# Performance work log

Hardware: AMD Instinct MI355X
Metric: run time of the kernel (lower is better)

Reference implementation:

```python
import jax, jax.numpy as jnp
import numpy as np

B, S, D, H = 2, 2048, 1024, 16
DK = D // H


def setup_inputs() -> dict:
    key = jax.random.key(0)
    ks = jax.random.split(key, 7)
    q = jax.random.normal(ks[0], (B, S, D), dtype=jnp.float32)
    k = jax.random.normal(ks[1], (B, S, D), dtype=jnp.float32)
    v = jax.random.normal(ks[2], (B, S, D), dtype=jnp.float32)
    # causal mask, broadcastable [B,1,S,S]; masked_fill where mask==0
    mask = jnp.broadcast_to(jnp.tril(jnp.ones((S, S), dtype=jnp.int32)), (B, 1, S, S))
    scale = 0.02
    Wq = jax.random.normal(ks[3], (D, D), dtype=jnp.float32) * scale
    Wk = jax.random.normal(ks[4], (D, D), dtype=jnp.float32) * scale
    Wv = jax.random.normal(ks[5], (D, D), dtype=jnp.float32) * scale
    Wo = jax.random.normal(ks[6], (D, D), dtype=jnp.float32) * scale
    return {"q": q, "k": k, "v": v, "mask": mask, "Wq": Wq, "Wk": Wk, "Wv": Wv, "Wo": Wo}


def reference(q, k, v, mask, Wq, Wk, Wv, Wo):
    # torch nn.Linear(bias=False): y = x @ W.T with W of shape [out, in]
    def proj(x, W):
        return (x @ W.T).reshape(B, S, H, DK).transpose(0, 2, 1, 3)  # [B,H,S,DK]

    Q = proj(q, Wq)
    K = proj(k, Wk)
    V = proj(v, Wv)
    inv_sqrt_dk = np.float32(1.0 / np.sqrt(DK))
    scores = jnp.einsum('bhqd,bhkd->bhqk', Q, K) * inv_sqrt_dk  # [B,H,S,S]
    scores = jnp.where(mask == 0, jnp.float32(-jnp.inf), scores)
    attn = jax.nn.softmax(scores, axis=-1)
    x = jnp.einsum('bhqk,bhkd->bhqd', attn, V)  # [B,H,S,DK]
    x = x.transpose(0, 2, 1, 3).reshape(B, S, D)
    return x @ Wo.T
```

## Files before the change

kernel.cpp:

```cpp
#include <hip/hip_runtime.h>

typedef __bf16 bf16x8 __attribute__((ext_vector_type(8)));
typedef __bf16 bf16x2 __attribute__((ext_vector_type(2)));
typedef float  f32x4  __attribute__((ext_vector_type(4)));

#define DEV static __device__ __forceinline__
#define VMCNT(n) asm volatile("s_waitcnt vmcnt(" #n ")" ::: "memory")
#define LGKM0()  asm volatile("s_waitcnt lgkmcnt(0)" ::: "memory")
#define SBAR()   __builtin_amdgcn_s_barrier()
#define SFENCE() __builtin_amdgcn_sched_barrier(0)


DEV ushort f2bf(float f) {
    return __builtin_bit_cast(ushort, (__bf16)f);
}
DEV uint pk2(float a, float b) {
    bf16x2 t; t[0] = (__bf16)a; t[1] = (__bf16)b;
    return __builtin_bit_cast(uint, t);
}

DEV float redmax4(float x) {
    x = fmaxf(x, __shfl_xor(x, 16));
    return fmaxf(x, __shfl_xor(x, 32));
}
DEV float redsum4(float x) {
    x += __shfl_xor(x, 16);
    return x + __shfl_xor(x, 32);
}

DEV void stage_swz(const ushort* g, int gstride, char* lds, int nchunks) {
    const int tid  = threadIdx.x;
    const int lane = tid & 63;
    const int wave = tid >> 6;
    for (int c0 = wave * 64; c0 < nchunks; c0 += 256) {
        int c   = c0 + lane;
        int row = c >> 3;
        int cc  = (c & 7) ^ (row & 7);
        const ushort* src = g + row * gstride + cc * 8;
        __builtin_amdgcn_global_load_lds((__attribute__((address_space(1))) void*)src,
                                         (__attribute__((address_space(3))) void*)(lds + c0 * 16),
                                         16, 0, 0);
    }
}

DEV void stage_swz32(const float* g, int gstride, char* lds, int nchunks) {
    const int tid  = threadIdx.x;
    const int lane = tid & 63;
    const int wave = tid >> 6;
    for (int c0 = wave * 64; c0 < nchunks; c0 += 256) {
        int c   = c0 + lane;
        int row = c >> 4;
        int cc  = (c & 15) ^ (row & 15);
        const float* src = g + row * gstride + cc * 4;
        __builtin_amdgcn_global_load_lds((__attribute__((address_space(1))) void*)src,
                                         (__attribute__((address_space(3))) void*)(lds + c0 * 16),
                                         16, 0, 0);
    }
}

DEV bf16x8 ldfrag(const char* tile, int row, int kc) {
    int off = (row << 7) + ((kc ^ (row & 7)) << 4);
    return *(const bf16x8*)(tile + off);
}

DEV bf16x8 ldfrag32(const char* tile, int row, int cl0) {
    const int base = row << 8, rs = row & 15;
    f32x4 v0 = *(const f32x4*)(tile + base + ((cl0 ^ rs) << 4));
    f32x4 v1 = *(const f32x4*)(tile + base + (((cl0 + 1) ^ rs) << 4));
    uint4 u;
    u.x = pk2(v0[0], v0[1]); u.y = pk2(v0[2], v0[3]);
    u.z = pk2(v1[0], v1[1]); u.w = pk2(v1[2], v1[3]);
    return __builtin_bit_cast(bf16x8, u);
}


struct CvtArgs { const float* s[4]; ushort* d[4]; int n; };

__global__ void cvt_kernel(CvtArgs a) {
    const float* __restrict__ s = a.s[blockIdx.y];
    ushort* __restrict__ d = a.d[blockIdx.y];
    const int stride = gridDim.x * blockDim.x;
    for (int i = blockIdx.x * blockDim.x + threadIdx.x; i * 8 < a.n; i += stride) {
        const float4* p = (const float4*)(s + (size_t)i * 8);
        float4 x = p[0], yv = p[1];
        uint4 o;
        o.x = pk2(x.x,  x.y);
        o.y = pk2(x.z,  x.w);
        o.z = pk2(yv.x, yv.y);
        o.w = pk2(yv.z, yv.w);
        *(uint4*)(d + (size_t)i * 8) = o;
    }
}

constexpr int GN = 1024, GK = 1024;


struct ProjArgs {
    const float* A[3]; const ushort* W[3]; ushort* O[3];
    float scale[3]; int mode[3];
};

__global__ __launch_bounds__(256, 3) void gemm_proj(ProjArgs args) {
    __shared__ char smem[49152];
    const int z = blockIdx.z;
    const float* A = args.A[z];
    const ushort* W = args.W[z];
    ushort* Out = args.O[z];
    const float scale = args.scale[z];
    const int mode = args.mode[z];

    const int tid  = threadIdx.x;
    const int lane = tid & 63;
    const int w    = tid >> 6;
    const int wr   = w >> 1, wc = w & 1;
    const int hi   = lane >> 4, lj = lane & 15;
    const int g    = blockIdx.x;
    const int o_   = ((g & 7) << 5) | (g >> 3);
    const int nb   = o_ & 7, mb = o_ >> 3;

    f32x4 acc[4][4];
#pragma unroll
    for (int mi = 0; mi < 4; mi++)
#pragma unroll
        for (int ni = 0; ni < 4; ni++) acc[mi][ni] = f32x4{0.f, 0.f, 0.f, 0.f};

    const float*  Ag = A + (size_t)mb * 128 * GK;
    const ushort* Wg = W + (size_t)nb * 128 * GK;

    for (int k0 = 0; k0 < GK; k0 += 64) {
        __syncthreads();
        stage_swz32(Ag + k0, GK, smem, 2048);
        stage_swz(Wg + k0, GK, smem + 32768, 1024);
        __syncthreads();
#pragma unroll
        for (int kk = 0; kk < 2; ++kk) {
            bf16x8 a[4], b[4];
#pragma unroll
            for (int mi = 0; mi < 4; mi++) a[mi] = ldfrag32(smem, wr * 64 + mi * 16 + lj, kk * 8 + hi * 2);
#pragma unroll
            for (int ni = 0; ni < 4; ni++) b[ni] = ldfrag(smem + 32768, wc * 64 + ni * 16 + lj, kk * 4 + hi);
#pragma unroll
            for (int mi = 0; mi < 4; mi++)
#pragma unroll
                for (int ni = 0; ni < 4; ni++)
                    acc[mi][ni] = __builtin_amdgcn_mfma_f32_16x16x32_bf16(a[mi], b[ni], acc[mi][ni], 0, 0, 0);
        }
    }

#pragma unroll
    for (int mi = 0; mi < 4; mi++)
#pragma unroll
        for (int r = 0; r < 4; r++) {
            const int gm = mb * 128 + wr * 64 + mi * 16 + hi * 4 + r;
            const int b_ = gm >> 11, s_ = gm & 2047;
#pragma unroll
            for (int ni = 0; ni < 4; ni++) {
                const int gn = nb * 128 + wc * 64 + ni * 16 + lj;
                const int h_ = gn >> 6, d_ = gn & 63;
                float v = acc[mi][ni][r] * scale;
                size_t off;
                if (mode == 0) off = (((size_t)b_ * 16 + h_) * 2048 + s_) * 64 + d_;
                else           off = (((size_t)b_ * 16 + h_) * 64 + d_) * 2048 + s_;
                Out[off] = f2bf(v);
            }
        }
}


__global__ __launch_bounds__(256, 3) void gemm_out(const ushort* __restrict__ A,
                                                   const ushort* __restrict__ W,
                                                   float* __restrict__ Out) {
    __shared__ char smem[32768];
    const int tid  = threadIdx.x;
    const int lane = tid & 63;
    const int w    = tid >> 6;
    const int wr   = w >> 1, wc = w & 1;
    const int hi   = lane >> 4, lj = lane & 15;
    const int g    = blockIdx.x;
    const int o_   = ((g & 7) << 5) | (g >> 3);
    const int nb   = o_ & 7, mb = o_ >> 3;

    f32x4 acc[4][4];
#pragma unroll
    for (int mi = 0; mi < 4; mi++)
#pragma unroll
        for (int ni = 0; ni < 4; ni++) acc[mi][ni] = f32x4{0.f, 0.f, 0.f, 0.f};

    const ushort* Ag = A + (size_t)mb * 128 * GK;
    const ushort* Wg = W + (size_t)nb * 128 * GK;

    for (int k0 = 0; k0 < GK; k0 += 64) {
        __syncthreads();
        stage_swz(Ag + k0, GK, smem, 1024);
        stage_swz(Wg + k0, GK, smem + 16384, 1024);
        __syncthreads();
#pragma unroll
        for (int kk = 0; kk < 2; ++kk) {
            bf16x8 a[4], b[4];
#pragma unroll
            for (int mi = 0; mi < 4; mi++) a[mi] = ldfrag(smem, wr * 64 + mi * 16 + lj, kk * 4 + hi);
#pragma unroll
            for (int ni = 0; ni < 4; ni++) b[ni] = ldfrag(smem + 16384, wc * 64 + ni * 16 + lj, kk * 4 + hi);
#pragma unroll
            for (int mi = 0; mi < 4; mi++)
#pragma unroll
                for (int ni = 0; ni < 4; ni++)
                    acc[mi][ni] = __builtin_amdgcn_mfma_f32_16x16x32_bf16(a[mi], b[ni], acc[mi][ni], 0, 0, 0);
        }
    }

#pragma unroll
    for (int mi = 0; mi < 4; mi++)
#pragma unroll
        for (int r = 0; r < 4; r++) {
            const int gm = mb * 128 + wr * 64 + mi * 16 + hi * 4 + r;
#pragma unroll
            for (int ni = 0; ni < 4; ni++) {
                const int gn = nb * 128 + wc * 64 + ni * 16 + lj;
                Out[(size_t)gm * GN + gn] = acc[mi][ni][r];
            }
        }
}


__global__ __launch_bounds__(256, 3) void attn_kernel(const ushort* __restrict__ Qb,
                                                      const ushort* __restrict__ Kb,
                                                      const ushort* __restrict__ Vt,
                                                      ushort* __restrict__ Xb,
                                                      ushort* __restrict__ Opart,
                                                      float* __restrict__ Mlp) {
    constexpr int S = 2048;
    __shared__ char smem[49152];
    const int tid = threadIdx.x, lane = tid & 63, w = tid >> 6;
    const int hi = lane >> 4, lj = lane & 15;
    char* Pw = smem + 32768 + w * 4096;
    const int bh = blockIdx.x;
    const int y = blockIdx.y;

    int qt, slice, nsl;
    if (y < 16)      { qt = 12 + (y & 3);            slice = y >> 2;        nsl = 4; }
    else if (y < 28) { int zz = y - 16; qt = 8 + (zz & 3); slice = zz >> 2; nsl = 3; }
    else if (y < 36) { int zz = y - 28; qt = 4 + (zz & 3); slice = zz >> 2; nsl = 2; }
    else             { qt = y - 36;                  slice = 0;             nsl = 1; }
    const int nt  = 2 * qt + 2;
    const int kts = (nt * slice) / nsl;
    const int kte = (nt * (slice + 1)) / nsl;
    const bool partial = (nsl > 1);

    const int q0 = qt * 128;
    const int q0w = q0 + w * 32;

    const ushort* Qg = Qb + (size_t)bh * S * 64;
    const ushort* Kg = Kb + (size_t)bh * S * 64;
    const ushort* Vg = Vt + (size_t)bh * 64 * S;

    bf16x8 qf[2][2];
#pragma unroll
    for (int mi = 0; mi < 2; mi++)
#pragma unroll
        for (int kk = 0; kk < 2; kk++)
            qf[mi][kk] = *(const bf16x8*)(Qg + (size_t)(q0w + mi * 16 + lj) * 64 + kk * 32 + hi * 8);

    f32x4 o[2][4];
    float m_run[2] = { -1e30f, -1e30f }, l_run[2] = { 0.f, 0.f };
#pragma unroll
    for (int mi = 0; mi < 2; mi++)
#pragma unroll
        for (int nd = 0; nd < 4; nd++) o[mi][nd] = f32x4{0.f, 0.f, 0.f, 0.f};

    stage_swz(Kg + (size_t)kts * 64 * 64, 64, smem, 512);
    stage_swz(Vg + kts * 64, S, smem + 16384, 512);
    int cur = 0;

    for (int t = kts; t < kte; ++t) {
        char* Kc = smem + (cur << 13);
        char* Vc = smem + 16384 + (cur << 13);
        if (t + 1 < kte) {
            stage_swz(Kg + (size_t)(t + 1) * 64 * 64, 64, smem + ((cur ^ 1) << 13), 512);
            stage_swz(Vg + (t + 1) * 64, S, smem + 16384 + ((cur ^ 1) << 13), 512);
            VMCNT(4);
        } else {
            VMCNT(0);
        }
        SBAR(); SFENCE();

        if (t * 64 <= q0w + 31) {
            f32x4 sc[2][4];
#pragma unroll
            for (int mi = 0; mi < 2; mi++)
#pragma unroll
                for (int ni = 0; ni < 4; ni++) sc[mi][ni] = f32x4{0.f, 0.f, 0.f, 0.f};
            __builtin_amdgcn_s_setprio(1);
#pragma unroll
            for (int kk = 0; kk < 2; ++kk) {
                bf16x8 kf[4];
#pragma unroll
                for (int ni = 0; ni < 4; ni++) kf[ni] = ldfrag(Kc, ni * 16 + lj, kk * 4 + hi);
#pragma unroll
                for (int mi = 0; mi < 2; mi++)
#pragma unroll
                    for (int ni = 0; ni < 4; ni++)
                        sc[mi][ni] = __builtin_amdgcn_mfma_f32_16x16x32_bf16(kf[ni], qf[mi][kk], sc[mi][ni], 0, 0, 0);
            }
            __builtin_amdgcn_s_setprio(0);

            const bool diag = (t * 64 + 63 > q0w);
#pragma unroll
            for (int mi = 0; mi < 2; mi++) {
                const int q = q0w + mi * 16 + lj;
                if (diag) {
#pragma unroll
                    for (int ni = 0; ni < 4; ni++)
#pragma unroll
                        for (int r = 0; r < 4; r++)
                            if (t * 64 + ni * 16 + hi * 4 + r > q) sc[mi][ni][r] = -1e30f;
                }
                float mx = -1e30f;
#pragma unroll
                for (int ni = 0; ni < 4; ni++)
#pragma unroll
                    for (int r = 0; r < 4; r++) mx = fmaxf(mx, sc[mi][ni][r]);
                mx = redmax4(mx);
                const float mo = m_run[mi];
                const bool defer = __all(mx <= mo + 8.f);
                float mn, rs;
                if (defer) { mn = mo; rs = 1.f; }
                else { mn = fmaxf(mo, mx); rs = __builtin_exp2f(mo - mn); m_run[mi] = mn; }
                float ps = 0.f;
                const int row = mi * 16 + lj;
#pragma unroll
                for (int ni = 0; ni < 4; ni++) {
                    float p0 = __builtin_exp2f(sc[mi][ni][0] - mn);
                    float p1 = __builtin_exp2f(sc[mi][ni][1] - mn);
                    float p2 = __builtin_exp2f(sc[mi][ni][2] - mn);
                    float p3 = __builtin_exp2f(sc[mi][ni][3] - mn);
                    ps += (p0 + p1) + (p2 + p3);
                    uint2 pv; pv.x = pk2(p0, p1); pv.y = pk2(p2, p3);
                    const int c = ni * 2 + (hi >> 1);
                    *(uint2*)(Pw + row * 128 + ((c ^ (row & 7)) << 4) + ((hi & 1) << 3)) = pv;
                }
                ps = redsum4(ps);
                if (defer) {
                    l_run[mi] += ps;
                } else {
                    l_run[mi] = l_run[mi] * rs + ps;
#pragma unroll
                    for (int r = 0; r < 4; r++) {
                        float rr = __shfl(rs, (lane & 48) | (hi * 4 + r));
#pragma unroll
                        for (int nd = 0; nd < 4; nd++) o[mi][nd][r] *= rr;
                    }
                }
            }

            LGKM0(); SFENCE();

            __builtin_amdgcn_s_setprio(1);
#pragma unroll
            for (int kk = 0; kk < 2; ++kk) {
                bf16x8 pa[2], bv[4];
#pragma unroll
                for (int mi = 0; mi < 2; mi++) pa[mi] = ldfrag(Pw, mi * 16 + lj, kk * 4 + hi);
#pragma unroll
                for (int nd = 0; nd < 4; nd++) bv[nd] = ldfrag(Vc, nd * 16 + lj, kk * 4 + hi);
#pragma unroll
                for (int mi = 0; mi < 2; mi++)
#pragma unroll
                    for (int nd = 0; nd < 4; nd++)
                        o[mi][nd] = __builtin_amdgcn_mfma_f32_16x16x32_bf16(pa[mi], bv[nd], o[mi][nd], 0, 0, 0);
            }
            __builtin_amdgcn_s_setprio(0);
        }

        LGKM0();
        SBAR(); SFENCE();
        cur ^= 1;
    }

    if (partial) {
        const int pidx = bh * 40 + y;
        ushort* Op = Opart + (size_t)pidx * 8192;
        float*  Ml = Mlp   + (size_t)pidx * 256;
#pragma unroll
        for (int mi = 0; mi < 2; mi++)
#pragma unroll
            for (int r = 0; r < 4; r++) {
                const int row = w * 32 + mi * 16 + hi * 4 + r;
#pragma unroll
                for (int nd = 0; nd < 4; nd++)
                    Op[row * 64 + nd * 16 + lj] = f2bf(o[mi][nd][r]);
            }
        if (hi == 0) {
#pragma unroll
            for (int mi = 0; mi < 2; mi++) {
                const int row = w * 32 + mi * 16 + lj;
                Ml[row * 2 + 0] = m_run[mi];
                Ml[row * 2 + 1] = l_run[mi];
            }
        }
    } else {
        const int b_ = bh >> 4, h_ = bh & 15;
#pragma unroll
        for (int mi = 0; mi < 2; mi++)
#pragma unroll
            for (int r = 0; r < 4; r++) {
                float lv = __shfl(l_run[mi], (lane & 48) | (hi * 4 + r));
                float inv = 1.f / lv;
                const int srow = q0w + mi * 16 + hi * 4 + r;
#pragma unroll
                for (int nd = 0; nd < 4; nd++)
                    Xb[((size_t)b_ * S + srow) * 1024 + h_ * 64 + nd * 16 + lj] =
                        f2bf(o[mi][nd][r] * inv);
            }
    }
}


__global__ __launch_bounds__(256) void attn_merge(const ushort* __restrict__ Op,
                                                  const float* __restrict__ Ml,
                                                  ushort* __restrict__ Xb) {
    const int bh = blockIdx.x;
    const int qt = 4 + blockIdx.y;
    const int nsl  = (qt < 8) ? 2 : (qt < 12) ? 3 : 4;
    const int ybase = (qt >= 12) ? (qt - 12) : (qt >= 8) ? (16 + qt - 8) : (28 + qt - 4);
    const int tid = threadIdx.x;
    const int row = tid >> 1;
    const int c0 = (tid & 1) * 32;

    float ms[4], ls[4];
    float m = -1e30f;
    for (int s = 0; s < nsl; ++s) {
        const int slot = bh * 40 + ybase + s * 4;
        ms[s] = Ml[(size_t)slot * 256 + row * 2 + 0];
        ls[s] = Ml[(size_t)slot * 256 + row * 2 + 1];
        m = fmaxf(m, ms[s]);
    }
    float acc[32];
#pragma unroll
    for (int c = 0; c < 32; ++c) acc[c] = 0.f;
    float l = 0.f;
    for (int s = 0; s < nsl; ++s) {
        const float a = __builtin_exp2f(ms[s] - m);
        l += ls[s] * a;
        const ushort* op = Op + (size_t)(bh * 40 + ybase + s * 4) * 8192 + row * 64 + c0;
#pragma unroll
        for (int c8 = 0; c8 < 32; c8 += 8) {
            bf16x8 v = *(const bf16x8*)(op + c8);
#pragma unroll
            for (int e = 0; e < 8; ++e) acc[c8 + e] += a * (float)v[e];
        }
    }
    const float inv = 1.f / l;
    const int b_ = bh >> 4, h_ = bh & 15;
    ushort* dst = Xb + ((size_t)b_ * 2048 + qt * 128 + row) * 1024 + h_ * 64 + c0;
#pragma unroll
    for (int c = 0; c < 32; c += 2)
        *(uint*)(dst + c) = pk2(acc[c] * inv, acc[c + 1] * inv);
}


extern "C" void kernel_launch(void* const* d_in, const int* in_sizes, int n_in,
                              void* d_out, int out_size, void* d_ws, size_t ws_size,
                              hipStream_t stream) {
    (void)in_sizes; (void)n_in; (void)out_size; (void)ws_size;
    const float* q  = (const float*)d_in[0];
    const float* k  = (const float*)d_in[1];
    const float* v  = (const float*)d_in[2];
    const float* Wq = (const float*)d_in[4];
    const float* Wk = (const float*)d_in[5];
    const float* Wv = (const float*)d_in[6];
    const float* Wo = (const float*)d_in[7];

    char* ws = (char*)d_ws;
    const size_t MB = (size_t)1 << 20;
    ushort* Qb   = (ushort*)(ws + 0 * MB);
    ushort* Kb   = (ushort*)(ws + 8 * MB);
    ushort* Vtb  = (ushort*)(ws + 16 * MB);
    ushort* Xb   = (ushort*)(ws + 24 * MB);
    ushort* Wqb  = (ushort*)(ws + 32 * MB);
    ushort* Wkb  = (ushort*)(ws + 34 * MB);
    ushort* Wvb  = (ushort*)(ws + 36 * MB);
    ushort* Wob  = (ushort*)(ws + 38 * MB);
    ushort* Opart= (ushort*)(ws + 40 * MB);
    float*  Mlp  = (float*) (ws + 60 * MB);

    CvtArgs c;
    c.s[0] = Wq;  c.s[1] = Wk;  c.s[2] = Wv;  c.s[3] = Wo;
    c.d[0] = Wqb; c.d[1] = Wkb; c.d[2] = Wvb; c.d[3] = Wob;
    c.n = 1024 * 1024;
    cvt_kernel<<<dim3(512, 4), 256, 0, stream>>>(c);

    ProjArgs p;
    p.A[0] = q;   p.A[1] = k;   p.A[2] = v;
    p.W[0] = Wqb; p.W[1] = Wkb; p.W[2] = Wvb;
    p.O[0] = Qb;  p.O[1] = Kb;  p.O[2] = Vtb;
    p.scale[0] = 0.125f * 1.44269504088896f;
    p.scale[1] = 1.0f; p.scale[2] = 1.0f;
    p.mode[0] = 0; p.mode[1] = 0; p.mode[2] = 1;
    gemm_proj<<<dim3(256, 1, 3), 256, 0, stream>>>(p);

    attn_kernel<<<dim3(32, 40), 256, 0, stream>>>(Qb, Kb, Vtb, Xb, Opart, Mlp);
    attn_merge<<<dim3(32, 12), 256, 0, stream>>>(Opart, Mlp, Xb);

    gemm_out<<<256, 256, 0, stream>>>(Xb, Wob, (float*)d_out);
}
```

Baseline: 248.3 us.

## Pre-convert activations to bf16 and halve output GEMM N-tile

```diff
diff --git a/kernel.cpp b/kernel.cpp
--- a/kernel.cpp
+++ b/kernel.cpp
@@ -43,44 +43,21 @@
     }
 }
 
-DEV void stage_swz32(const float* g, int gstride, char* lds, int nchunks) {
-    const int tid  = threadIdx.x;
-    const int lane = tid & 63;
-    const int wave = tid >> 6;
-    for (int c0 = wave * 64; c0 < nchunks; c0 += 256) {
-        int c   = c0 + lane;
-        int row = c >> 4;
-        int cc  = (c & 15) ^ (row & 15);
-        const float* src = g + row * gstride + cc * 4;
-        __builtin_amdgcn_global_load_lds((__attribute__((address_space(1))) void*)src,
-                                         (__attribute__((address_space(3))) void*)(lds + c0 * 16),
-                                         16, 0, 0);
-    }
-}
-
 DEV bf16x8 ldfrag(const char* tile, int row, int kc) {
     int off = (row << 7) + ((kc ^ (row & 7)) << 4);
     return *(const bf16x8*)(tile + off);
 }
 
-DEV bf16x8 ldfrag32(const char* tile, int row, int cl0) {
-    const int base = row << 8, rs = row & 15;
-    f32x4 v0 = *(const f32x4*)(tile + base + ((cl0 ^ rs) << 4));
-    f32x4 v1 = *(const f32x4*)(tile + base + (((cl0 + 1) ^ rs) << 4));
-    uint4 u;
-    u.x = pk2(v0[0], v0[1]); u.y = pk2(v0[2], v0[3]);
-    u.z = pk2(v1[0], v1[1]); u.w = pk2(v1[2], v1[3]);
-    return __builtin_bit_cast(bf16x8, u);
-}
-
-
-struct CvtArgs { const float* s[4]; ushort* d[4]; int n; };
+
+struct CvtArgs { const float* s[7]; ushort* d[7]; int n[7]; };
 
 __global__ void cvt_kernel(CvtArgs a) {
-    const float* __restrict__ s = a.s[blockIdx.y];
-    ushort* __restrict__ d = a.d[blockIdx.y];
+    const int y = blockIdx.y;
+    const float* __restrict__ s = a.s[y];
+    ushort* __restrict__ d = a.d[y];
+    const int n = a.n[y];
     const int stride = gridDim.x * blockDim.x;
-    for (int i = blockIdx.x * blockDim.x + threadIdx.x; i * 8 < a.n; i += stride) {
+    for (int i = blockIdx.x * blockDim.x + threadIdx.x; i * 8 < n; i += stride) {
         const float4* p = (const float4*)(s + (size_t)i * 8);
         float4 x = p[0], yv = p[1];
         uint4 o;
@@ -96,14 +73,14 @@
 
 
 struct ProjArgs {
-    const float* A[3]; const ushort* W[3]; ushort* O[3];
+    const ushort* A[3]; const ushort* W[3]; ushort* O[3];
     float scale[3]; int mode[3];
 };
 
 __global__ __launch_bounds__(256, 3) void gemm_proj(ProjArgs args) {
-    __shared__ char smem[49152];
+    __shared__ char smem[32768];
     const int z = blockIdx.z;
-    const float* A = args.A[z];
+    const ushort* A = args.A[z];
     const ushort* W = args.W[z];
     ushort* Out = args.O[z];
     const float scale = args.scale[z];
@@ -124,21 +101,21 @@
 #pragma unroll
         for (int ni = 0; ni < 4; ni++) acc[mi][ni] = f32x4{0.f, 0.f, 0.f, 0.f};
 
-    const float*  Ag = A + (size_t)mb * 128 * GK;
+    const ushort* Ag = A + (size_t)mb * 128 * GK;
     const ushort* Wg = W + (size_t)nb * 128 * GK;
 
     for (int k0 = 0; k0 < GK; k0 += 64) {
         __syncthreads();
-        stage_swz32(Ag + k0, GK, smem, 2048);
-        stage_swz(Wg + k0, GK, smem + 32768, 1024);
+        stage_swz(Ag + k0, GK, smem, 1024);
+        stage_swz(Wg + k0, GK, smem + 16384, 1024);
         __syncthreads();
 #pragma unroll
         for (int kk = 0; kk < 2; ++kk) {
             bf16x8 a[4], b[4];
 #pragma unroll
-            for (int mi = 0; mi < 4; mi++) a[mi] = ldfrag32(smem, wr * 64 + mi * 16 + lj, kk * 8 + hi * 2);
-#pragma unroll
-            for (int ni = 0; ni < 4; ni++) b[ni] = ldfrag(smem + 32768, wc * 64 + ni * 16 + lj, kk * 4 + hi);
+            for (int mi = 0; mi < 4; mi++) a[mi] = ldfrag(smem, wr * 64 + mi * 16 + lj, kk * 4 + hi);
+#pragma unroll
+            for (int ni = 0; ni < 4; ni++) b[ni] = ldfrag(smem + 16384, wc * 64 + ni * 16 + lj, kk * 4 + hi);
 #pragma unroll
             for (int mi = 0; mi < 4; mi++)
 #pragma unroll
@@ -170,41 +147,41 @@
 __global__ __launch_bounds__(256, 3) void gemm_out(const ushort* __restrict__ A,
                                                    const ushort* __restrict__ W,
                                                    float* __restrict__ Out) {
-    __shared__ char smem[32768];
+    __shared__ char smem[24576];
     const int tid  = threadIdx.x;
     const int lane = tid & 63;
     const int w    = tid >> 6;
     const int wr   = w >> 1, wc = w & 1;
     const int hi   = lane >> 4, lj = lane & 15;
     const int g    = blockIdx.x;
-    const int o_   = ((g & 7) << 5) | (g >> 3);
-    const int nb   = o_ & 7, mb = o_ >> 3;
-
-    f32x4 acc[4][4];
+    const int o_   = ((g & 7) << 6) | (g >> 3);
+    const int nb   = o_ & 15, mb = o_ >> 4;
+
+    f32x4 acc[4][2];
 #pragma unroll
     for (int mi = 0; mi < 4; mi++)
 #pragma unroll
-        for (int ni = 0; ni < 4; ni++) acc[mi][ni] = f32x4{0.f, 0.f, 0.f, 0.f};
+        for (int ni = 0; ni < 2; ni++) acc[mi][ni] = f32x4{0.f, 0.f, 0.f, 0.f};
 
     const ushort* Ag = A + (size_t)mb * 128 * GK;
-    const ushort* Wg = W + (size_t)nb * 128 * GK;
+    const ushort* Wg = W + (size_t)nb * 64 * GK;
 
     for (int k0 = 0; k0 < GK; k0 += 64) {
         __syncthreads();
         stage_swz(Ag + k0, GK, smem, 1024);
-        stage_swz(Wg + k0, GK, smem + 16384, 1024);
+        stage_swz(Wg + k0, GK, smem + 16384, 512);
         __syncthreads();
 #pragma unroll
         for (int kk = 0; kk < 2; ++kk) {
-            bf16x8 a[4], b[4];
+            bf16x8 a[4], b[2];
 #pragma unroll
             for (int mi = 0; mi < 4; mi++) a[mi] = ldfrag(smem, wr * 64 + mi * 16 + lj, kk * 4 + hi);
 #pragma unroll
-            for (int ni = 0; ni < 4; ni++) b[ni] = ldfrag(smem + 16384, wc * 64 + ni * 16 + lj, kk * 4 + hi);
+            for (int ni = 0; ni < 2; ni++) b[ni] = ldfrag(smem + 16384, wc * 32 + ni * 16 + lj, kk * 4 + hi);
 #pragma unroll
             for (int mi = 0; mi < 4; mi++)
 #pragma unroll
-                for (int ni = 0; ni < 4; ni++)
+                for (int ni = 0; ni < 2; ni++)
                     acc[mi][ni] = __builtin_amdgcn_mfma_f32_16x16x32_bf16(a[mi], b[ni], acc[mi][ni], 0, 0, 0);
         }
     }
@@ -215,8 +192,8 @@
         for (int r = 0; r < 4; r++) {
             const int gm = mb * 128 + wr * 64 + mi * 16 + hi * 4 + r;
 #pragma unroll
-            for (int ni = 0; ni < 4; ni++) {
-                const int gn = nb * 128 + wc * 64 + ni * 16 + lj;
+            for (int ni = 0; ni < 2; ni++) {
+                const int gn = nb * 64 + wc * 32 + ni * 16 + lj;
                 Out[(size_t)gm * GN + gn] = acc[mi][ni][r];
             }
         }
@@ -477,21 +454,25 @@
     ushort* Kb   = (ushort*)(ws + 8 * MB);
     ushort* Vtb  = (ushort*)(ws + 16 * MB);
     ushort* Xb   = (ushort*)(ws + 24 * MB);
-    ushort* Wqb  = (ushort*)(ws + 32 * MB);
-    ushort* Wkb  = (ushort*)(ws + 34 * MB);
-    ushort* Wvb  = (ushort*)(ws + 36 * MB);
-    ushort* Wob  = (ushort*)(ws + 38 * MB);
-    ushort* Opart= (ushort*)(ws + 40 * MB);
-    float*  Mlp  = (float*) (ws + 60 * MB);
+    ushort* qb   = (ushort*)(ws + 32 * MB);
+    ushort* kb   = (ushort*)(ws + 40 * MB);
+    ushort* vb   = (ushort*)(ws + 48 * MB);
+    ushort* Wqb  = (ushort*)(ws + 56 * MB);
+    ushort* Wkb  = (ushort*)(ws + 58 * MB);
+    ushort* Wvb  = (ushort*)(ws + 60 * MB);
+    ushort* Wob  = (ushort*)(ws + 62 * MB);
+    ushort* Opart= (ushort*)(ws + 32 * MB);
+    float*  Mlp  = (float*) (ws + 52 * MB);
 
     CvtArgs c;
-    c.s[0] = Wq;  c.s[1] = Wk;  c.s[2] = Wv;  c.s[3] = Wo;
-    c.d[0] = Wqb; c.d[1] = Wkb; c.d[2] = Wvb; c.d[3] = Wob;
-    c.n = 1024 * 1024;
-    cvt_kernel<<<dim3(512, 4), 256, 0, stream>>>(c);
+    c.s[0] = q;  c.s[1] = k;  c.s[2] = v;  c.s[3] = Wq;  c.s[4] = Wk;  c.s[5] = Wv;  c.s[6] = Wo;
+    c.d[0] = qb; c.d[1] = kb; c.d[2] = vb; c.d[3] = Wqb; c.d[4] = Wkb; c.d[5] = Wvb; c.d[6] = Wob;
+    c.n[0] = c.n[1] = c.n[2] = 4 * 1024 * 1024;
+    c.n[3] = c.n[4] = c.n[5] = c.n[6] = 1024 * 1024;
+    cvt_kernel<<<dim3(1024, 7), 256, 0, stream>>>(c);
 
     ProjArgs p;
-    p.A[0] = q;   p.A[1] = k;   p.A[2] = v;
+    p.A[0] = qb;  p.A[1] = kb;  p.A[2] = vb;
     p.W[0] = Wqb; p.W[1] = Wkb; p.W[2] = Wvb;
     p.O[0] = Qb;  p.O[1] = Kb;  p.O[2] = Vtb;
     p.scale[0] = 0.125f * 1.44269504088896f;
@@ -502,5 +483,5 @@
     attn_kernel<<<dim3(32, 40), 256, 0, stream>>>(Qb, Kb, Vtb, Xb, Opart, Mlp);
     attn_merge<<<dim3(32, 12), 256, 0, stream>>>(Opart, Mlp, Xb);
 
-    gemm_out<<<256, 256, 0, stream>>>(Xb, Wob, (float*)d_out);
-}
+    gemm_out<<<512, 256, 0, stream>>>(Xb, Wob, (float*)d_out);
+}
```

Result: faster. 237.9 us (-4.2%).
